# Kernel tuning notes

Measured on AMD Instinct MI355X. Metric: run time of the kernel, lower is better.

The kernel has to match this reference:

```python
import jax, jax.numpy as jnp
import numpy as np

NEG = -1e9

def setup_inputs() -> dict:
    key = jax.random.key(0)
    k1, k2, k3 = jax.random.split(key, 3)
    B, C_len, Q_len, H = 32, 1024, 128, 512
    C = jax.random.normal(k1, (B, C_len, H), dtype=jnp.float32)
    Q = jax.random.normal(k2, (B, Q_len, H), dtype=jnp.float32)
    q_mask = jnp.ones((B, Q_len), dtype=jnp.int32)
    # sim.weight of nn.Linear(3H, 1, bias=False), flattened: [w1 | w2 | w3]
    w = jax.random.normal(k3, (3 * H,), dtype=jnp.float32) * (1.0 / np.sqrt(3 * H))
    return {"C": C, "Q": Q, "q_mask": q_mask, "w": w}

def reference(C, Q, q_mask, w):
    B, C_len, H = C.shape
    w1, w2, w3 = w[:H], w[H:2 * H], w[2 * H:]
    # Trilinear similarity: S[b,i,j] = C[b,i].w1 + Q[b,j].w2 + sum_h C[b,i,h]*Q[b,j,h]*w3[h]
    s_c = C @ w1                                   # [B, C_len]
    s_q = Q @ w2                                   # [B, Q_len]
    s_cq = jnp.einsum('bih,bjh->bij', C * w3, Q)   # [B, C_len, Q_len]
    S = s_cq + s_c[:, :, None] + s_q[:, None, :]
    S = jnp.where(q_mask[:, None, :] == 0, NEG, S)
    # Context-to-query attention
    A = jax.nn.softmax(S, axis=-1) @ Q             # [B, C_len, H]
    # Query-to-context attention
    maxS = S.max(axis=-1)                          # [B, C_len]
    B_att = jax.nn.softmax(maxS, axis=-1)          # [B, C_len]
    B_vec = jnp.einsum('bi,bih->bh', B_att, C)     # [B, H]
    B_vec = jnp.broadcast_to(B_vec[:, None, :], (B, C_len, H))
    return jnp.concatenate([C, A, C * A, C * B_vec], axis=-1)
```

## Files before the change

### kernel.cpp

```cpp
#include <hip/hip_runtime.h>
#include <stdint.h>

#define NEGV (-1000000000.0f)

typedef float  f32x4  __attribute__((ext_vector_type(4)));
typedef __bf16 bf16x8 __attribute__((ext_vector_type(8)));

__device__ __forceinline__ unsigned short f2bf(float f){
  union { float f; unsigned u; } v; v.f = f;
  unsigned r = v.u + 0x7FFFu + ((v.u >> 16) & 1u);
  return (unsigned short)(r >> 16);
}
__device__ __forceinline__ unsigned packbf2(float a, float b){
  return (unsigned)f2bf(a) | ((unsigned)f2bf(b) << 16);
}
__device__ __forceinline__ void gl_lds16(const void* g, const char* l){
  __builtin_amdgcn_global_load_lds(
      (const __attribute__((address_space(1))) void*)g,
      (__attribute__((address_space(3))) void*)(unsigned)(uintptr_t)l,
      16, 0, 0);
}


__global__ __launch_bounds__(256) void k0_prep(const float* __restrict__ Q,
                                               const float* __restrict__ w,
                                               char* __restrict__ qbf,
                                               char* __restrict__ qtbf,
                                               float* __restrict__ sq_part)
{
  __shared__ float tile[128][129];
  __shared__ float sqs[128];
  const int bid = blockIdx.x, t = threadIdx.x;
  const int b = bid >> 2, hc = bid & 3;
  if (t < 128) sqs[t] = 0.f;
  __syncthreads();
  for (int it = 0; it < 16; ++it){
    int idx = it*256 + t;
    int j = idx >> 5, h4 = idx & 31;
    const f32x4 q4 = *(const f32x4*)(Q + ((size_t)b*128 + j)*512 + hc*128 + h4*4);
    *(f32x4*)(&tile[j][h4*4]) = q4;
    unsigned lo = packbf2(q4.x, q4.y), hi = packbf2(q4.z, q4.w);
    int k = hc*128 + h4*4;
    int o = (k >> 6)*16384 + ((j*128 + (k & 63)*2) ^ ((j & 7) << 4));
    char* dst = qbf + (size_t)b*131072 + o;
    *(unsigned*)dst = lo; *(unsigned*)(dst + 4) = hi;
    const float* w2 = w + 512 + k;
    float p = q4.x*w2[0] + q4.y*w2[1] + q4.z*w2[2] + q4.w*w2[3];
    for (int s = 16; s > 0; s >>= 1) p += __shfl_down(p, s, 32);
    if ((t & 31) == 0) sqs[j] += p;
  }
  __syncthreads();
  for (int it = 0; it < 32; ++it){
    int idx = it*256 + t;
    int hr = idx >> 6, j2 = idx & 63;
    float a = tile[j2*2][hr], c = tile[j2*2+1][hr];
    int h = hc*128 + hr;
    int o = (h >> 6)*16384 + (((h & 63)*256 + j2*4) ^ ((h & 7) << 4));
    *(unsigned*)(qtbf + (size_t)b*131072 + o) = packbf2(a, c);
  }
  if (t < 128) sq_part[(size_t)(b*4 + hc)*128 + t] = sqs[t];
}

__global__ __launch_bounds__(512, 4) void k1_main(
    const float* __restrict__ C, const int* __restrict__ qmask,
    const float* __restrict__ w, const float* __restrict__ sq_part,
    const char* __restrict__ qbf, const char* __restrict__ qtbf,
    float* __restrict__ out, float* __restrict__ num_part,
    float* __restrict__ den_part)
{
  __shared__ __align__(16) char lds_c[65536];
  __shared__ __align__(16) char cw[8192];
  __shared__ float w1l[512], w3l[512];
  __shared__ float sqf[128];
  __shared__ int   msk[128];
  __shared__ float exf[32];
  __shared__ float mh[4][32], sh[4][32];

  const int t = threadIdx.x;
  const int bid = blockIdx.x;
  const int xcd = bid & 7, jj = bid >> 3;
  const int b = xcd*4 + (jj >> 5), itile = jj & 31;
  const int i0 = itile * 32;
  const int wv = t >> 6, ln = t & 63;
  const int jq = wv & 3;
  const int ihalf = wv >> 2;
  const int g = ln >> 4, c16 = ln & 15;
  const int iloc = ihalf*16 + c16;

  {
    const char* ctile = (const char*)(C + (size_t)(b*1024 + i0)*512);
    #pragma unroll
    for (int r = 0; r < 8; ++r){
      const int ob  = wv*8192 + r*1024;
      const int row = ob >> 11;
      const int msw = ((row & 7) << 4) | (((row >> 3) & 1) << 7);
      gl_lds16(ctile + ob + ((ln << 4) ^ msw), lds_c + ob);
    }
  }
  if (t < 128){
    sqf[t] = sq_part[(size_t)(b*4 + 0)*128 + t] + sq_part[(size_t)(b*4 + 1)*128 + t]
           + sq_part[(size_t)(b*4 + 2)*128 + t] + sq_part[(size_t)(b*4 + 3)*128 + t];
    msk[t] = qmask[b*128 + t];
  }
  w1l[t] = w[t];
  w3l[t] = w[1024 + t];
  __syncthreads();

  const char* qsrc  = qbf  + (size_t)b * 131072;
  const char* qtsrc = qtbf + (size_t)b * 131072;
  const size_t rowb = (size_t)(b*1024 + i0 + iloc);
  const int swz = ((iloc & 7) << 4) | (((iloc >> 3) & 1) << 7);

  float scp = 0.f;
  f32x4 acc[2] = {};
  #pragma unroll
  for (int ch = 0; ch < 8; ++ch){
    #pragma unroll
    for (int ks = 0; ks < 2; ++ks){
      const int k0 = ch*64 + ks*32 + g*8;
      const int lo = iloc*2048 + k0*4;
      const f32x4 cA  = *(const f32x4*)(lds_c + (lo ^ swz));
      const f32x4 cB  = *(const f32x4*)(lds_c + ((lo + 16) ^ swz));
      const f32x4 w3A = *(const f32x4*)(w3l + k0);
      const f32x4 w3B = *(const f32x4*)(w3l + k0 + 4);
      const f32x4 w1A = *(const f32x4*)(w1l + k0);
      const f32x4 w1B = *(const f32x4*)(w1l + k0 + 4);
      scp += cA.x*w1A.x + cA.y*w1A.y + cA.z*w1A.z + cA.w*w1A.w
           + cB.x*w1B.x + cB.y*w1B.y + cB.z*w1B.z + cB.w*w1B.w;
      bf16x8 bv;
      bv[0] = (__bf16)(cA.x*w3A.x); bv[1] = (__bf16)(cA.y*w3A.y);
      bv[2] = (__bf16)(cA.z*w3A.z); bv[3] = (__bf16)(cA.w*w3A.w);
      bv[4] = (__bf16)(cB.x*w3B.x); bv[5] = (__bf16)(cB.y*w3B.y);
      bv[6] = (__bf16)(cB.z*w3B.z); bv[7] = (__bf16)(cB.w*w3B.w);
      const int kb = ks*64 + g*16;
      #pragma unroll
      for (int mf = 0; mf < 2; ++mf){
        int j = (jq*2 + mf)*16 + c16;
        bf16x8 av = *(const bf16x8*)(qsrc + ch*16384 + ((j*128 + kb) ^ ((j & 7) << 4)));
        acc[mf] = __builtin_amdgcn_mfma_f32_16x16x32_bf16(av, bv, acc[mf], 0, 0, 0);
      }
    }
  }
  scp += __shfl_xor(scp, 16);
  scp += __shfl_xor(scp, 32);
  const float sc = scp;

  float m = -3.0e38f;
  #pragma unroll
  for (int mf = 0; mf < 2; ++mf)
    #pragma unroll
    for (int r = 0; r < 4; ++r){
      int j = (jq*2 + mf)*16 + g*4 + r;
      float v = msk[j] ? (acc[mf][r] + sc + sqf[j]) : NEGV;
      acc[mf][r] = v;
      m = fmaxf(m, v);
    }
  m = fmaxf(m, __shfl_xor(m, 16));
  m = fmaxf(m, __shfl_xor(m, 32));
  float s = 0.f;
  #pragma unroll
  for (int mf = 0; mf < 2; ++mf)
    #pragma unroll
    for (int r = 0; r < 4; ++r){
      float e = __expf(acc[mf][r] - m);
      acc[mf][r] = e; s += e;
    }
  s += __shfl_xor(s, 16);
  s += __shfl_xor(s, 32);
  if (g == 0){ mh[jq][iloc] = m; sh[jq][iloc] = s; }
  __syncthreads();

  const float m01 = fmaxf(mh[0][iloc], mh[1][iloc]);
  const float m23 = fmaxf(mh[2][iloc], mh[3][iloc]);
  const float mF  = fmaxf(m01, m23);
  const float sF  = sh[0][iloc]*__expf(mh[0][iloc] - mF)
                  + sh[1][iloc]*__expf(mh[1][iloc] - mF)
                  + sh[2][iloc]*__expf(mh[2][iloc] - mF)
                  + sh[3][iloc]*__expf(mh[3][iloc] - mF);
  const float scale = __expf(m - mF) / sF;
  #pragma unroll
  for (int mf = 0; mf < 2; ++mf){
    uint64_t pk = (uint64_t)packbf2(acc[mf][0]*scale, acc[mf][1]*scale)
                | ((uint64_t)packbf2(acc[mf][2]*scale, acc[mf][3]*scale) << 32);
    *(uint64_t*)(cw + ((iloc*256 + (jq*2 + mf)*32 + g*8) ^ ((iloc & 7) << 4))) = pk;
  }
  if (jq == 0 && g == 0) exf[iloc] = __expf(mF);
  __syncthreads();

  bf16x8 pb[4];
  #pragma unroll
  for (int ks = 0; ks < 4; ++ks)
    pb[ks] = *(const bf16x8*)(cw + ((iloc*256 + ks*64 + g*16) ^ ((iloc & 7) << 4)));

  #pragma unroll
  for (int hc2 = 0; hc2 < 2; ++hc2){
    const int hch = jq*2 + hc2;
    f32x4 a2[4] = {};
    #pragma unroll
    for (int nf = 0; nf < 4; ++nf){
      int hr = nf*16 + c16;
      #pragma unroll
      for (int ks = 0; ks < 4; ++ks){
        bf16x8 qa = *(const bf16x8*)(qtsrc + hch*16384 +
                        ((hr*256 + ks*64 + g*16) ^ ((hr & 7) << 4)));
        a2[nf] = __builtin_amdgcn_mfma_f32_16x16x32_bf16(qa, pb[ks], a2[nf], 0, 0, 0);
      }
    }
    #pragma unroll
    for (int nf = 0; nf < 4; ++nf){
      int h = hch*64 + nf*16 + g*4;
      const int lo = iloc*2048 + h*4;
      const f32x4 c4 = *(const f32x4*)(lds_c + (lo ^ swz));
      f32x4 av = a2[nf];
      *(f32x4*)(out + rowb*2048 + h)        = c4;
      *(f32x4*)(out + rowb*2048 + 512 + h)  = av;
      f32x4 ca = av * c4;
      *(f32x4*)(out + rowb*2048 + 1024 + h) = ca;
    }
  }


  float n0 = 0.f;
  #pragma unroll 8
  for (int i2 = 0; i2 < 32; ++i2){
    const int ms = ((i2 & 7) << 4) | (((i2 >> 3) & 1) << 7);
    n0 += exf[i2] * *(const float*)(lds_c + ((i2*2048 + t*4) ^ ms));
  }
  num_part[((size_t)(b*32 + itile))*512 + t] = n0;
  if (t < 32){
    float d = exf[t];
    for (int s2 = 16; s2 > 0; s2 >>= 1) d += __shfl_down(d, s2, 32);
    if (t == 0) den_part[b*32 + itile] = d;
  }
}

__global__ __launch_bounds__(256) void k2_bvec(const float* __restrict__ num_part,
                                               const float* __restrict__ den_part,
                                               float* __restrict__ bvec)
{
  int b = blockIdx.x, t = threadIdx.x;
  float d = 0.f;
  for (int k = 0; k < 32; ++k) d += den_part[b*32 + k];
  float inv = 1.0f / d;
  for (int h = t; h < 512; h += 256){
    float s = 0.f;
    for (int k = 0; k < 32; ++k) s += num_part[(size_t)(b*32 + k)*512 + h];
    bvec[b*512 + h] = s * inv;
  }
}

__global__ __launch_bounds__(256) void k3_cout(const float* __restrict__ C,
                                               const float* __restrict__ bvec,
                                               float* __restrict__ out)
{
  int t = threadIdx.x;
  size_t row = (size_t)blockIdx.x*2 + (t >> 7);
  int col4 = t & 127;
  int b = (int)(row >> 10);
  const f32x4 c4 = *(const f32x4*)(C + row*512 + col4*4);
  const f32x4 bv = *(const f32x4*)(bvec + (size_t)b*512 + col4*4);
  f32x4 cb;
  cb.x = c4.x*bv.x; cb.y = c4.y*bv.y; cb.z = c4.z*bv.z; cb.w = c4.w*bv.w;
  *(f32x4*)(out + row*2048 + 1536 + col4*4) = cb;
}

extern "C" void kernel_launch(void* const* d_in, const int* in_sizes, int n_in,
                              void* d_out, int out_size, void* d_ws, size_t ws_size,
                              hipStream_t stream)
{
  const float* C     = (const float*)d_in[0];
  const float* Q     = (const float*)d_in[1];
  const int*   qmask = (const int*)d_in[2];
  const float* w     = (const float*)d_in[3];
  float* out = (float*)d_out;
  char*  ws  = (char*)d_ws;

  char*  qbf      = ws;
  char*  qtbf     = ws + (4 << 20);
  float* sq_part  = (float*)(ws + (8 << 20));
  float* num_part = (float*)(ws + (8 << 20) + (1 << 16));
  float* den_part = (float*)(ws + (10 << 20) + (1 << 16));
  float* bvec     = (float*)(ws + (10 << 20) + (1 << 16) + 8192);

  k0_prep<<<128, 256, 0, stream>>>(Q, w, qbf, qtbf, sq_part);
  k1_main<<<1024, 512, 0, stream>>>(C, qmask, w, sq_part, qbf, qtbf,
                                    out, num_part, den_part);
  k2_bvec<<<32, 256, 0, stream>>>(num_part, den_part, bvec);
  k3_cout<<<16384, 256, 0, stream>>>(C, bvec, out);
}
```

Baseline: 121.9 us.

## Halve k1 row tile to 16 rows with 8 waves each owning a query slice

The main kernel now processes 16 context rows per block instead of 32. Each of the 8 waves owns one 16-column query slice for the score GEMM and one 64-wide H chunk for the attention GEMM. LDS use drops by about half and launch bounds go from 4 to 6 blocks per SM, raising occupancy, while the grid doubles to 2048 blocks and the partial-sum buffers grow to 64 tiles per batch. In exchange, each Q fragment load from global/L2 is reused across fewer rows, so L2 traffic for the Q operands roughly doubles.

```diff
diff --git a/kernel.cpp b/kernel.cpp
--- a/kernel.cpp
+++ b/kernel.cpp
@@ -61,37 +61,35 @@
   if (t < 128) sq_part[(size_t)(b*4 + hc)*128 + t] = sqs[t];
 }
 
-__global__ __launch_bounds__(512, 4) void k1_main(
+__global__ __launch_bounds__(512, 6) void k1_main(
     const float* __restrict__ C, const int* __restrict__ qmask,
     const float* __restrict__ w, const float* __restrict__ sq_part,
     const char* __restrict__ qbf, const char* __restrict__ qtbf,
     float* __restrict__ out, float* __restrict__ num_part,
     float* __restrict__ den_part)
 {
-  __shared__ __align__(16) char lds_c[65536];
-  __shared__ __align__(16) char cw[8192];
+  __shared__ __align__(16) char lds_c[32768];
+  __shared__ __align__(16) char cw[4096];
   __shared__ float w1l[512], w3l[512];
   __shared__ float sqf[128];
   __shared__ int   msk[128];
-  __shared__ float exf[32];
-  __shared__ float mh[4][32], sh[4][32];
+  __shared__ float exf[16];
+  __shared__ float mh[8][16], sh[8][16];
 
   const int t = threadIdx.x;
   const int bid = blockIdx.x;
   const int xcd = bid & 7, jj = bid >> 3;
-  const int b = xcd*4 + (jj >> 5), itile = jj & 31;
-  const int i0 = itile * 32;
+  const int b = xcd*4 + (jj >> 6), itile = jj & 63;
+  const int i0 = itile * 16;
   const int wv = t >> 6, ln = t & 63;
-  const int jq = wv & 3;
-  const int ihalf = wv >> 2;
   const int g = ln >> 4, c16 = ln & 15;
-  const int iloc = ihalf*16 + c16;
+  const int iloc = c16;
 
   {
     const char* ctile = (const char*)(C + (size_t)(b*1024 + i0)*512);
     #pragma unroll
-    for (int r = 0; r < 8; ++r){
-      const int ob  = wv*8192 + r*1024;
+    for (int r = 0; r < 4; ++r){
+      const int ob  = wv*4096 + r*1024;
       const int row = ob >> 11;
       const int msw = ((row & 7) << 4) | (((row >> 3) & 1) << 7);
       gl_lds16(ctile + ob + ((ln << 4) ^ msw), lds_c + ob);
@@ -112,7 +110,7 @@
   const int swz = ((iloc & 7) << 4) | (((iloc >> 3) & 1) << 7);
 
   float scp = 0.f;
-  f32x4 acc[2] = {};
+  f32x4 acc = {};
   #pragma unroll
   for (int ch = 0; ch < 8; ++ch){
     #pragma unroll
@@ -133,12 +131,9 @@
       bv[4] = (__bf16)(cB.x*w3B.x); bv[5] = (__bf16)(cB.y*w3B.y);
       bv[6] = (__bf16)(cB.z*w3B.z); bv[7] = (__bf16)(cB.w*w3B.w);
       const int kb = ks*64 + g*16;
-      #pragma unroll
-      for (int mf = 0; mf < 2; ++mf){
-        int j = (jq*2 + mf)*16 + c16;
-        bf16x8 av = *(const bf16x8*)(qsrc + ch*16384 + ((j*128 + kb) ^ ((j & 7) << 4)));
-        acc[mf] = __builtin_amdgcn_mfma_f32_16x16x32_bf16(av, bv, acc[mf], 0, 0, 0);
-      }
+      const int j = wv*16 + c16;
+      bf16x8 av = *(const bf16x8*)(qsrc + ch*16384 + ((j*128 + kb) ^ ((j & 7) << 4)));
+      acc = __builtin_amdgcn_mfma_f32_16x16x32_bf16(av, bv, acc, 0, 0, 0);
     }
   }
   scp += __shfl_xor(scp, 16);
@@ -147,44 +142,38 @@
 
   float m = -3.0e38f;
   #pragma unroll
-  for (int mf = 0; mf < 2; ++mf)
-    #pragma unroll
-    for (int r = 0; r < 4; ++r){
-      int j = (jq*2 + mf)*16 + g*4 + r;
-      float v = msk[j] ? (acc[mf][r] + sc + sqf[j]) : NEGV;
-      acc[mf][r] = v;
-      m = fmaxf(m, v);
-    }
+  for (int r = 0; r < 4; ++r){
+    int j = wv*16 + g*4 + r;
+    float v = msk[j] ? (acc[r] + sc + sqf[j]) : NEGV;
+    acc[r] = v;
+    m = fmaxf(m, v);
+  }
   m = fmaxf(m, __shfl_xor(m, 16));
   m = fmaxf(m, __shfl_xor(m, 32));
   float s = 0.f;
   #pragma unroll
-  for (int mf = 0; mf < 2; ++mf)
-    #pragma unroll
-    for (int r = 0; r < 4; ++r){
-      float e = __expf(acc[mf][r] - m);
-      acc[mf][r] = e; s += e;
-    }
+  for (int r = 0; r < 4; ++r){
+    float e = __expf(acc[r] - m);
+    acc[r] = e; s += e;
+  }
   s += __shfl_xor(s, 16);
   s += __shfl_xor(s, 32);
-  if (g == 0){ mh[jq][iloc] = m; sh[jq][iloc] = s; }
-  __syncthreads();
-
-  const float m01 = fmaxf(mh[0][iloc], mh[1][iloc]);
-  const float m23 = fmaxf(mh[2][iloc], mh[3][iloc]);
-  const float mF  = fmaxf(m01, m23);
-  const float sF  = sh[0][iloc]*__expf(mh[0][iloc] - mF)
-                  + sh[1][iloc]*__expf(mh[1][iloc] - mF)
-                  + sh[2][iloc]*__expf(mh[2][iloc] - mF)
-                  + sh[3][iloc]*__expf(mh[3][iloc] - mF);
+  if (g == 0){ mh[wv][iloc] = m; sh[wv][iloc] = s; }
+  __syncthreads();
+
+  float mF = mh[0][iloc];
+  #pragma unroll
+  for (int q = 1; q < 8; ++q) mF = fmaxf(mF, mh[q][iloc]);
+  float sF = 0.f;
+  #pragma unroll
+  for (int q = 0; q < 8; ++q) sF += sh[q][iloc]*__expf(mh[q][iloc] - mF);
   const float scale = __expf(m - mF) / sF;
-  #pragma unroll
-  for (int mf = 0; mf < 2; ++mf){
-    uint64_t pk = (uint64_t)packbf2(acc[mf][0]*scale, acc[mf][1]*scale)
-                | ((uint64_t)packbf2(acc[mf][2]*scale, acc[mf][3]*scale) << 32);
-    *(uint64_t*)(cw + ((iloc*256 + (jq*2 + mf)*32 + g*8) ^ ((iloc & 7) << 4))) = pk;
-  }
-  if (jq == 0 && g == 0) exf[iloc] = __expf(mF);
+  {
+    uint64_t pk = (uint64_t)packbf2(acc[0]*scale, acc[1]*scale)
+                | ((uint64_t)packbf2(acc[2]*scale, acc[3]*scale) << 32);
+    *(uint64_t*)(cw + ((iloc*256 + wv*32 + g*8) ^ ((iloc & 7) << 4))) = pk;
+  }
+  if (wv == 0 && g == 0) exf[iloc] = __expf(mF);
   __syncthreads();
 
   bf16x8 pb[4];
@@ -192,45 +181,42 @@
   for (int ks = 0; ks < 4; ++ks)
     pb[ks] = *(const bf16x8*)(cw + ((iloc*256 + ks*64 + g*16) ^ ((iloc & 7) << 4)));
 
-  #pragma unroll
-  for (int hc2 = 0; hc2 < 2; ++hc2){
-    const int hch = jq*2 + hc2;
-    f32x4 a2[4] = {};
+  f32x4 a2[4] = {};
+  #pragma unroll
+  for (int nf = 0; nf < 4; ++nf){
+    int hr = nf*16 + c16;
     #pragma unroll
-    for (int nf = 0; nf < 4; ++nf){
-      int hr = nf*16 + c16;
-      #pragma unroll
-      for (int ks = 0; ks < 4; ++ks){
-        bf16x8 qa = *(const bf16x8*)(qtsrc + hch*16384 +
-                        ((hr*256 + ks*64 + g*16) ^ ((hr & 7) << 4)));
-        a2[nf] = __builtin_amdgcn_mfma_f32_16x16x32_bf16(qa, pb[ks], a2[nf], 0, 0, 0);
-      }
+    for (int ks = 0; ks < 4; ++ks){
+      bf16x8 qa = *(const bf16x8*)(qtsrc + wv*16384 +
+                      ((hr*256 + ks*64 + g*16) ^ ((hr & 7) << 4)));
+      a2[nf] = __builtin_amdgcn_mfma_f32_16x16x32_bf16(qa, pb[ks], a2[nf], 0, 0, 0);
     }
-    #pragma unroll
-    for (int nf = 0; nf < 4; ++nf){
-      int h = hch*64 + nf*16 + g*4;
-      const int lo = iloc*2048 + h*4;
-      const f32x4 c4 = *(const f32x4*)(lds_c + (lo ^ swz));
-      f32x4 av = a2[nf];
-      *(f32x4*)(out + rowb*2048 + h)        = c4;
-      *(f32x4*)(out + rowb*2048 + 512 + h)  = av;
-      f32x4 ca = av * c4;
-      *(f32x4*)(out + rowb*2048 + 1024 + h) = ca;
-    }
+  }
+  #pragma unroll
+  for (int nf = 0; nf < 4; ++nf){
+    int h = wv*64 + nf*16 + g*4;
+    const int lo = iloc*2048 + h*4;
+    const f32x4 c4 = *(const f32x4*)(lds_c + (lo ^ swz));
+    f32x4 av = a2[nf];
+    *(f32x4*)(out + rowb*2048 + h)        = c4;
+    *(f32x4*)(out + rowb*2048 + 512 + h)  = av;
+    f32x4 ca = av * c4;
+    *(f32x4*)(out + rowb*2048 + 1024 + h) = ca;
   }
 
 
   float n0 = 0.f;
-  #pragma unroll 8
-  for (int i2 = 0; i2 < 32; ++i2){
+  #pragma unroll
+  for (int i2 = 0; i2 < 16; ++i2){
     const int ms = ((i2 & 7) << 4) | (((i2 >> 3) & 1) << 7);
     n0 += exf[i2] * *(const float*)(lds_c + ((i2*2048 + t*4) ^ ms));
   }
-  num_part[((size_t)(b*32 + itile))*512 + t] = n0;
-  if (t < 32){
+  num_part[((size_t)(b*64 + itile))*512 + t] = n0;
+  if (t < 16){
     float d = exf[t];
-    for (int s2 = 16; s2 > 0; s2 >>= 1) d += __shfl_down(d, s2, 32);
-    if (t == 0) den_part[b*32 + itile] = d;
+    d += __shfl_down(d, 8, 16); d += __shfl_down(d, 4, 16);
+    d += __shfl_down(d, 2, 16); d += __shfl_down(d, 1, 16);
+    if (t == 0) den_part[b*64 + itile] = d;
   }
 }
 
@@ -240,11 +226,11 @@
 {
   int b = blockIdx.x, t = threadIdx.x;
   float d = 0.f;
-  for (int k = 0; k < 32; ++k) d += den_part[b*32 + k];
+  for (int k = 0; k < 64; ++k) d += den_part[b*64 + k];
   float inv = 1.0f / d;
   for (int h = t; h < 512; h += 256){
     float s = 0.f;
-    for (int k = 0; k < 32; ++k) s += num_part[(size_t)(b*32 + k)*512 + h];
+    for (int k = 0; k < 64; ++k) s += num_part[(size_t)(b*64 + k)*512 + h];
     bvec[b*512 + h] = s * inv;
   }
 }
@@ -279,11 +265,11 @@
   char*  qtbf     = ws + (4 << 20);
   float* sq_part  = (float*)(ws + (8 << 20));
   float* num_part = (float*)(ws + (8 << 20) + (1 << 16));
-  float* den_part = (float*)(ws + (10 << 20) + (1 << 16));
-  float* bvec     = (float*)(ws + (10 << 20) + (1 << 16) + 8192);
+  float* den_part = (float*)(ws + (12 << 20) + (1 << 16));
+  float* bvec     = (float*)(ws + (12 << 20) + (1 << 16) + 8192);
 
   k0_prep<<<128, 256, 0, stream>>>(Q, w, qbf, qtbf, sq_part);
-  k1_main<<<1024, 512, 0, stream>>>(C, qmask, w, sq_part, qbf, qtbf,
+  k1_main<<<2048, 512, 0, stream>>>(C, qmask, w, sq_part, qbf, qtbf,
                                     out, num_part, den_part);
   k2_bvec<<<32, 256, 0, stream>>>(num_part, den_part, bvec);
   k3_cout<<<16384, 256, 0, stream>>>(C, bvec, out);
```

Measured after the change: 122.0 us. Within noise of the previous version (+0.1%).
